# Kernel optimization log

Measured on AMD Instinct MI355X. Metric: run time of the kernel, lower is better.

## Reference

```python
import jax, jax.numpy as jnp
import numpy as np

WS = 7          # window size
SHIFT = 3       # shift size (SW-MSA)
NH = 4          # num heads
EPS = 1e-5      # LayerNorm eps (torch default)


def _rel_pos_index(ws):
    coords = np.stack(np.meshgrid(np.arange(ws), np.arange(ws), indexing='ij'))  # (2, ws, ws)
    cf = coords.reshape(2, -1)                      # (2, ws*ws)
    rel = cf[:, :, None] - cf[:, None, :]           # (2, N, N)
    rel = rel.transpose(1, 2, 0)
    rel[:, :, 0] += ws - 1
    rel[:, :, 1] += ws - 1
    rel[:, :, 0] *= 2 * ws - 1
    return jnp.asarray(rel.sum(-1))                 # (N, N) int

REL_IDX = _rel_pos_index(WS)


def _shift_mask(Hp, Wp, ws, shift):
    """Standard Swin attention mask for shifted windows: (nW, N, N) float32."""
    img = np.zeros((1, Hp, Wp, 1), dtype=np.float32)
    cnt = 0
    sl = (slice(0, -ws), slice(-ws, -shift), slice(-shift, None))
    for h in sl:
        for w in sl:
            img[:, h, w, :] = cnt
            cnt += 1
    win = img.reshape(1, Hp // ws, ws, Wp // ws, ws, 1).transpose(0, 1, 3, 2, 4, 5)
    win = win.reshape(-1, ws * ws)                  # (nW, N)
    m = win[:, None, :] - win[:, :, None]
    return jnp.asarray(np.where(m != 0, -100.0, 0.0).astype(np.float32))


def _ln(x, g, b):
    mu = jnp.mean(x, -1, keepdims=True)
    var = jnp.mean(jnp.square(x - mu), -1, keepdims=True)
    return (x - mu) * jax.lax.rsqrt(var + EPS) * g + b


def _win_partition(x, ws):
    B, H, W, C = x.shape
    x = x.reshape(B, H // ws, ws, W // ws, ws, C).transpose(0, 1, 3, 2, 4, 5)
    return x.reshape(-1, ws * ws, C)


def _win_reverse(w, ws, B, H, W):
    C = w.shape[-1]
    x = w.reshape(B, H // ws, W // ws, ws, ws, C).transpose(0, 1, 3, 2, 4, 5)
    return x.reshape(B, H, W, C)


def setup_inputs() -> dict:
    key = jax.random.key(0)
    ks = jax.random.split(key, 12)
    B, H, W, C = 16, 112, 112, 128
    hid = 4 * C
    std = 0.02
    inp = {
        'x': jax.random.normal(ks[0], (B, H * W, C), jnp.float32),
        'H': H, 'W': W,
        'attn_mask': _shift_mask(H, W, WS, SHIFT),
        'ln1_g': jnp.ones((C,), jnp.float32),
        'ln1_b': jnp.zeros((C,), jnp.float32),
        'qkv_w': jax.random.normal(ks[1], (3 * C, C), jnp.float32) * std,
        'qkv_b': jnp.zeros((3 * C,), jnp.float32),
        'rel_bias_table': jax.random.normal(ks[2], ((2 * WS - 1) ** 2, NH), jnp.float32) * std,
        'proj_w': jax.random.normal(ks[3], (C, C), jnp.float32) * std,
        'proj_b': jnp.zeros((C,), jnp.float32),
        'ln2_g': jnp.ones((C,), jnp.float32),
        'ln2_b': jnp.zeros((C,), jnp.float32),
        'fc1_w': jax.random.normal(ks[4], (hid, C), jnp.float32) * std,
        'fc1_b': jnp.zeros((hid,), jnp.float32),
        'fc2_w': jax.random.normal(ks[5], (C, hid), jnp.float32) * std,
        'fc2_b': jnp.zeros((C,), jnp.float32),
    }
    return inp


def reference(x, H, W, attn_mask, ln1_g, ln1_b, qkv_w, qkv_b, rel_bias_table,
              proj_w, proj_b, ln2_g, ln2_b, fc1_w, fc1_b, fc2_w, fc2_b):
    B, L, C = x.shape
    N = WS * WS
    hd = C // NH
    scale = hd ** -0.5

    shortcut = x
    h = _ln(x, ln1_g, ln1_b).reshape(B, H, W, C)
    # H, W chosen divisible by WS -> no padding branch needed
    h = jnp.roll(h, shift=(-SHIFT, -SHIFT), axis=(1, 2))
    xw = _win_partition(h, WS)                      # (B_, N, C), B_ = B*nW
    B_ = xw.shape[0]
    nW = attn_mask.shape[0]

    qkv = xw @ qkv_w.T + qkv_b                      # (B_, N, 3C)
    qkv = qkv.reshape(B_, N, 3, NH, hd).transpose(2, 0, 3, 1, 4)
    q, k, v = qkv[0], qkv[1], qkv[2]                # (B_, NH, N, hd)

    attn = jnp.einsum('bhnd,bhmd->bhnm', q, k) * scale
    bias = rel_bias_table[REL_IDX]                  # (N, N, NH)
    attn = attn + bias.transpose(2, 0, 1)[None]     # (B_, NH, N, N)
    attn = attn.reshape(B_ // nW, nW, NH, N, N) + attn_mask[None, :, None]
    attn = jax.nn.softmax(attn.reshape(B_, NH, N, N), axis=-1)

    o = jnp.einsum('bhnm,bhmd->bhnd', attn, v)      # (B_, NH, N, hd)
    o = o.transpose(0, 2, 1, 3).reshape(B_, N, C)
    o = o @ proj_w.T + proj_b

    h = _win_reverse(o, WS, B, H, W)
    h = jnp.roll(h, shift=(SHIFT, SHIFT), axis=(1, 2))
    x1 = shortcut + h.reshape(B, L, C)

    f = _ln(x1, ln2_g, ln2_b)
    f = jax.nn.gelu(f @ fc1_w.T + fc1_b, approximate=False)
    f = f @ fc2_w.T + fc2_b
    return x1 + f
```

## Files before the change

### kernel.cpp

```cpp
#include <hip/hip_runtime.h>
#include <hip/hip_bf16.h>
#include <math.h>

#define B_IMG 16
#define HH 112
#define WW_ 112
#define CC 128
#define LL (HH*WW_)
#define BWIN 4096
#define NTOK 49
#define NROWS (BWIN*NTOK)
#define HD 32
#define SCALE 0.1767766952966369f
#define SHIFT_ 3

typedef short bf16x8 __attribute__((ext_vector_type(8)));
typedef float f32x4 __attribute__((ext_vector_type(4)));
typedef unsigned short ushort_t;

__device__ __forceinline__ float wave_sum(float v) {
#pragma unroll
  for (int off = 32; off >= 1; off >>= 1) v += __shfl_xor(v, off, 64);
  return v;
}

__global__ __launch_bounds__(256) void castw_kernel(const float* __restrict__ w,
                                                    __hip_bfloat16* __restrict__ o, int n) {
  int i = blockIdx.x * 256 + threadIdx.x;
  if (i < n) o[i] = __float2bfloat16(w[i]);
}

__global__ __launch_bounds__(256) void prep_bias(const float* __restrict__ table,
                                                 float* __restrict__ biasPad) {
  int idx = blockIdx.x * 256 + threadIdx.x;
  int h = idx >> 12, q = (idx >> 6) & 63, k = idx & 63;
  float v = 0.f;
  if (q < NTOK && k < NTOK) {
    int yi = q / 7, xi = q % 7, yj = k / 7, xj = k % 7;
    v = table[((yi - yj + 6) * 13 + (xi - xj + 6)) * 4 + h];
  }
  biasPad[idx] = v;
}

__global__ __launch_bounds__(256) void prep_mask(const float* __restrict__ mask,
                                                 float* __restrict__ maskPad) {
  int idx = blockIdx.x * 256 + threadIdx.x;
  int pat = idx >> 12, q = (idx >> 6) & 63, k = idx & 63;
  float v = -1e30f;
  if (q < NTOK && k < NTOK) v = mask[pat * (NTOK * NTOK) + q * NTOK + k];
  maskPad[idx] = v;
}

template<bool GATHER>
__global__ __launch_bounds__(256) void ln_kernel(
    const float* __restrict__ X, const float* __restrict__ g,
    const float* __restrict__ b, __hip_bfloat16* __restrict__ Y)
{
  int wid  = threadIdx.x >> 6;
  int lane = threadIdx.x & 63;
  int r = blockIdx.x * 4 + wid;
  size_t src;
  if (GATHER) {
    int win = r / NTOK, n = r % NTOK;
    int bi = win >> 8, wi = win & 255;
    int wh = wi >> 4, wwi = wi & 15;
    int ii = n / 7, jj = n % 7;
    int hp = wh * 7 + ii, wp = wwi * 7 + jj;
    int sh = (hp + SHIFT_) % HH, sw = (wp + SHIFT_) % WW_;
    src = ((size_t)bi * LL + (size_t)sh * WW_ + sw) * CC;
  } else {
    src = (size_t)r * CC;
  }
  float v0 = X[src + lane];
  float v1 = X[src + 64 + lane];
  float mean = wave_sum(v0 + v1) * (1.f / CC);
  float d0 = v0 - mean, d1 = v1 - mean;
  float var = wave_sum(d0 * d0 + d1 * d1) * (1.f / CC);
  float rstd = rsqrtf(var + 1e-5f);
  size_t dst = (size_t)r * CC;
  Y[dst + lane]      = __float2bfloat16(d0 * rstd * g[lane]      + b[lane]);
  Y[dst + 64 + lane] = __float2bfloat16(d1 * rstd * g[lane + 64] + b[lane + 64]);
}

enum { EPI_BIAS = 0, EPI_GELU = 1, EPI_RES = 2, EPI_PROJ = 3 };
#define LDSW 136

#define STAGE_A(KB)                                                              \
  _Pragma("unroll")                                                              \
  for (int p = 0; p < 8; ++p) {                                                  \
    int lin = p * 256 + t;                                                       \
    int row = lin >> 4;                                                          \
    int col = (lin & 15) * 8;                                                    \
    *(uint4*)&As[row * LDSW + col] =                                             \
        *(const uint4*)(A + (size_t)(m0 + row) * K + (KB) + col);                \
  }

#define STAGE_B(NOFF, KB)                                                        \
  _Pragma("unroll")                                                              \
  for (int p = 0; p < 8; ++p) {                                                  \
    int lin = p * 256 + t;                                                       \
    int row = lin >> 4;                                                          \
    int col = (lin & 15) * 8;                                                    \
    *(uint4*)&Bs[row * LDSW + col] =                                             \
        *(const uint4*)(W + (size_t)((NOFF) + row) * K + (KB) + col);            \
  }

#define MFMA_BLOCK                                                               \
  _Pragma("unroll")                                                              \
  for (int ks = 0; ks < 4; ++ks) {                                               \
    int k0 = ks * 32 + quad * 8;                                                 \
    bf16x8 af[4], bf[4];                                                         \
    _Pragma("unroll")                                                            \
    for (int i = 0; i < 4; ++i)                                                  \
      af[i] = *(const bf16x8*)&As[(wr + i * 16 + l16) * LDSW + k0];              \
    _Pragma("unroll")                                                            \
    for (int j = 0; j < 4; ++j)                                                  \
      bf[j] = *(const bf16x8*)&Bs[(wc + j * 16 + l16) * LDSW + k0];              \
    _Pragma("unroll")                                                            \
    for (int i = 0; i < 4; ++i)                                                  \
      _Pragma("unroll")                                                          \
      for (int j = 0; j < 4; ++j)                                                \
        acc[i][j] = __builtin_amdgcn_mfma_f32_16x16x32_bf16(af[i], bf[j],        \
                                                            acc[i][j], 0, 0, 0); \
  }

template<int EPI, int NB, bool LNF>
__global__ __launch_bounds__(256, 2) void gemm_bf16(
    const ushort_t* __restrict__ A, const ushort_t* __restrict__ W,
    const float* __restrict__ bias, const float* __restrict__ aux,
    void* __restrict__ outp, const float* __restrict__ g2,
    const float* __restrict__ b2, __hip_bfloat16* __restrict__ ln_out,
    int N, int K)
{
  __shared__ ushort_t As[128 * LDSW];
  __shared__ ushort_t Bs[128 * LDSW];
  int t = threadIdx.x;
  int lane = t & 63;
  int quad = lane >> 4;
  int l16  = lane & 15;
  int wr = (t >> 7) * 64;
  int wc = ((t >> 6) & 1) * 64;
  int m0 = blockIdx.x * 128;

  f32x4 acc[4][4];

  for (int nb = 0; nb < NB; ++nb) {
    int n_off = (NB == 1) ? blockIdx.y * 128 : nb * 128;
#pragma unroll
    for (int i = 0; i < 4; ++i)
#pragma unroll
      for (int j = 0; j < 4; ++j) acc[i][j] = (f32x4){0.f, 0.f, 0.f, 0.f};

    if (NB == 1) {
      for (int kb = 0; kb < K; kb += 128) {
        if (kb) __syncthreads();
        STAGE_A(kb);
        STAGE_B(n_off, kb);
        __syncthreads();
        MFMA_BLOCK;
      }
    } else {
      if (nb == 0) { STAGE_A(0); STAGE_B(0, 0); }
      __syncthreads();
      MFMA_BLOCK;
      __syncthreads();
      if (nb + 1 < NB) { STAGE_B((nb + 1) * 128, 0); }
    }

    if (EPI == EPI_PROJ) {
      float s[4][4], ss[4][4];
      unsigned rowB[4][4];
#pragma unroll
      for (int i = 0; i < 4; ++i) {
#pragma unroll
        for (int r = 0; r < 4; ++r) {
          s[i][r] = 0.f; ss[i][r] = 0.f;
          int m = m0 + wr + i * 16 + quad * 4 + r;
          int win = m / NTOK, nn = m % NTOK;
          int bi = win >> 8, wi = win & 255;
          int wh = wi >> 4, wwi = wi & 15;
          int ii = nn / 7, jj = nn % 7;
          int hp = wh * 7 + ii, wp = wwi * 7 + jj;
          int oh = (hp + SHIFT_) % HH, ow = (wp + SHIFT_) % WW_;
          unsigned base = ((unsigned)bi * LL + (unsigned)oh * WW_ + ow) * CC;
          rowB[i][r] = base;
#pragma unroll
          for (int j = 0; j < 4; ++j) {
            int n = wc + j * 16 + l16;
            float x1 = aux[base + n] + acc[i][j][r] + bias[n];
            ((float*)outp)[base + n] = x1;
            if (LNF) {
              acc[i][j][r] = x1;
              s[i][r] += x1;
              ss[i][r] = fmaf(x1, x1, ss[i][r]);
            }
          }
        }
      }
      if (LNF) {
#pragma unroll
        for (int i = 0; i < 4; ++i)
#pragma unroll
          for (int r = 0; r < 4; ++r) {
#pragma unroll
            for (int off = 8; off >= 1; off >>= 1) {
              s[i][r]  += __shfl_xor(s[i][r],  off, 64);
              ss[i][r] += __shfl_xor(ss[i][r], off, 64);
            }
          }
        float* red = (float*)As;
        __syncthreads();
        if (l16 == 0) {
#pragma unroll
          for (int i = 0; i < 4; ++i)
#pragma unroll
            for (int r = 0; r < 4; ++r) {
              int ml = wr + i * 16 + quad * 4 + r;
              red[((wc >> 6) * 128 + ml) * 2 + 0] = s[i][r];
              red[((wc >> 6) * 128 + ml) * 2 + 1] = ss[i][r];
            }
        }
        __syncthreads();
#pragma unroll
        for (int i = 0; i < 4; ++i)
#pragma unroll
          for (int r = 0; r < 4; ++r) {
            int ml = wr + i * 16 + quad * 4 + r;
            float st  = red[ml * 2 + 0] + red[(128 + ml) * 2 + 0];
            float sst = red[ml * 2 + 1] + red[(128 + ml) * 2 + 1];
            float mean = st * (1.f / 128.f);
            float var  = sst * (1.f / 128.f) - mean * mean;
            s[i][r]  = mean;
            ss[i][r] = rsqrtf(var + 1e-5f);
          }
#pragma unroll
        for (int i = 0; i < 4; ++i)
#pragma unroll
          for (int r = 0; r < 4; ++r) {
            unsigned base = rowB[i][r];
#pragma unroll
            for (int j = 0; j < 4; ++j) {
              int n = wc + j * 16 + l16;
              float ln = (acc[i][j][r] - s[i][r]) * ss[i][r] * g2[n] + b2[n];
              ln_out[(size_t)base + n] = __float2bfloat16(ln);
            }
          }
      }
    } else {
#pragma unroll
      for (int i = 0; i < 4; ++i) {
#pragma unroll
        for (int j = 0; j < 4; ++j) {
          int n = n_off + wc + j * 16 + l16;
          float bn = bias[n];
#pragma unroll
          for (int reg = 0; reg < 4; ++reg) {
            int m = m0 + wr + i * 16 + quad * 4 + reg;
            float v = acc[i][j][reg] + bn;
            if (EPI == EPI_BIAS) {
              ((__hip_bfloat16*)outp)[(size_t)m * N + n] = __float2bfloat16(v);
            } else if (EPI == EPI_GELU) {
              v = 0.5f * v * (1.f + erff(v * 0.70710678118654752f));
              ((__hip_bfloat16*)outp)[(size_t)m * N + n] = __float2bfloat16(v);
            } else {
              ((float*)outp)[(size_t)m * N + n] = v + aux[(size_t)m * N + n];
            }
          }
        }
      }
    }
  }
}

#define WLDS 6656

__global__ __launch_bounds__(256) void attn_mfma(
    const ushort_t* __restrict__ qkv, const float* __restrict__ maskPad,
    const float* __restrict__ biasPad, __hip_bfloat16* __restrict__ O, int win_off)
{
  __shared__ ushort_t lds[4 * WLDS];
  const int win_l = blockIdx.x;
  const int win_g = win_off + win_l;
  const int h    = threadIdx.x >> 6;
  const int lane = threadIdx.x & 63;
  const int quad = lane >> 4;
  const int l16  = lane & 15;
  ushort_t* wb = lds + h * WLDS;
  ushort_t* Vt = wb + 4608;

  {
    const int tok = lane;
    uint4 z = make_uint4(0u, 0u, 0u, 0u);
    uint4 k0 = z, k1 = z, k2 = z, k3 = z;
    union { uint4 v4[4]; ushort_t u[32]; } vv;
    vv.v4[0] = z; vv.v4[1] = z; vv.v4[2] = z; vv.v4[3] = z;
    if (tok < NTOK) {
      const ushort_t* src = qkv + ((size_t)win_l * NTOK + tok) * 384 + h * HD;
      k0 = *(const uint4*)(src + 128); k1 = *(const uint4*)(src + 136);
      k2 = *(const uint4*)(src + 144); k3 = *(const uint4*)(src + 152);
      vv.v4[0] = *(const uint4*)(src + 256); vv.v4[1] = *(const uint4*)(src + 264);
      vv.v4[2] = *(const uint4*)(src + 272); vv.v4[3] = *(const uint4*)(src + 280);
    }
    *(uint4*)&wb[tok * 40 +  0] = k0;
    *(uint4*)&wb[tok * 40 +  8] = k1;
    *(uint4*)&wb[tok * 40 + 16] = k2;
    *(uint4*)&wb[tok * 40 + 24] = k3;
#pragma unroll
    for (int d = 0; d < 32; ++d) Vt[d * 64 + tok] = vv.u[d];
  }

  bf16x8 qf[4];
  {
    const ushort_t* qb = qkv + (size_t)win_l * NTOK * 384 + h * HD + quad * 8;
#pragma unroll
    for (int i = 0; i < 4; ++i)
      qf[i] = *(const bf16x8*)(qb + (size_t)(i * 16 + l16) * 384);
  }

  f32x4 S[4][4];
#pragma unroll
  for (int i = 0; i < 4; ++i)
#pragma unroll
    for (int j = 0; j < 4; ++j) S[i][j] = (f32x4){0.f, 0.f, 0.f, 0.f};
  bf16x8 kf[4];
#pragma unroll
  for (int j = 0; j < 4; ++j)
    kf[j] = *(const bf16x8*)&wb[(j * 16 + l16) * 40 + quad * 8];
#pragma unroll
  for (int i = 0; i < 4; ++i)
#pragma unroll
    for (int j = 0; j < 4; ++j)
      S[i][j] = __builtin_amdgcn_mfma_f32_16x16x32_bf16(qf[i], kf[j], S[i][j], 0, 0, 0);

  const float* mrow = maskPad + (size_t)(win_g & 255) * 4096;
  const float* brow = biasPad + (size_t)h * 4096;
#pragma unroll
  for (int i = 0; i < 4; ++i)
#pragma unroll
    for (int j = 0; j < 4; ++j)
#pragma unroll
      for (int r = 0; r < 4; ++r) {
        int q = i * 16 + quad * 4 + r;
        int k = j * 16 + l16;
        S[i][j][r] = fmaf(S[i][j][r], SCALE, brow[q * 64 + k] + mrow[q * 64 + k]);
      }

  float inv[4][4];
#pragma unroll
  for (int i = 0; i < 4; ++i)
#pragma unroll
    for (int r = 0; r < 4; ++r) {
      float mx = fmaxf(fmaxf(S[i][0][r], S[i][1][r]), fmaxf(S[i][2][r], S[i][3][r]));
      mx = fmaxf(mx, __shfl_xor(mx, 1, 64));
      mx = fmaxf(mx, __shfl_xor(mx, 2, 64));
      mx = fmaxf(mx, __shfl_xor(mx, 4, 64));
      mx = fmaxf(mx, __shfl_xor(mx, 8, 64));
      float sum = 0.f;
#pragma unroll
      for (int j = 0; j < 4; ++j) {
        float e = __expf(S[i][j][r] - mx);
        S[i][j][r] = e;
        sum += e;
      }
      sum += __shfl_xor(sum, 1, 64);
      sum += __shfl_xor(sum, 2, 64);
      sum += __shfl_xor(sum, 4, 64);
      sum += __shfl_xor(sum, 8, 64);
      inv[i][r] = 1.f / sum;
    }

#pragma unroll
  for (int i = 0; i < 4; ++i)
#pragma unroll
    for (int j = 0; j < 4; ++j)
#pragma unroll
      for (int r = 0; r < 4; ++r) {
        int q = i * 16 + quad * 4 + r;
        int k = j * 16 + l16;
        *(__hip_bfloat16*)&wb[q * 72 + k] = __float2bfloat16(S[i][j][r]);
      }

  f32x4 Oacc[4][2];
#pragma unroll
  for (int i = 0; i < 4; ++i) {
    Oacc[i][0] = (f32x4){0.f, 0.f, 0.f, 0.f};
    Oacc[i][1] = (f32x4){0.f, 0.f, 0.f, 0.f};
  }
  bf16x8 vf[2][2];
#pragma unroll
  for (int ks = 0; ks < 2; ++ks)
#pragma unroll
    for (int jp = 0; jp < 2; ++jp)
      vf[ks][jp] = *(const bf16x8*)&Vt[(jp * 16 + l16) * 64 + ks * 32 + quad * 8];
#pragma unroll
  for (int i = 0; i < 4; ++i)
#pragma unroll
    for (int ks = 0; ks < 2; ++ks) {
      bf16x8 pf = *(const bf16x8*)&wb[(i * 16 + l16) * 72 + ks * 32 + quad * 8];
#pragma unroll
      for (int jp = 0; jp < 2; ++jp)
        Oacc[i][jp] = __builtin_amdgcn_mfma_f32_16x16x32_bf16(pf, vf[ks][jp], Oacc[i][jp], 0, 0, 0);
    }

  __hip_bfloat16* ob = O + ((size_t)win_g * NTOK) * CC + h * HD;
#pragma unroll
  for (int i = 0; i < 4; ++i)
#pragma unroll
    for (int r = 0; r < 4; ++r) {
      int q = i * 16 + quad * 4 + r;
      if (q < NTOK) {
        float sc = inv[i][r];
#pragma unroll
        for (int jp = 0; jp < 2; ++jp)
          ob[(size_t)q * CC + jp * 16 + l16] = __float2bfloat16(Oacc[i][jp][r] * sc);
      }
    }
}

extern "C" void kernel_launch(void* const* d_in, const int* in_sizes, int n_in,
                              void* d_out, int out_size, void* d_ws, size_t ws_size,
                              hipStream_t stream) {
  const float* x        = (const float*)d_in[0];
  const float* attnmask = (const float*)d_in[3];
  const float* ln1_g    = (const float*)d_in[4];
  const float* ln1_b    = (const float*)d_in[5];
  const float* qkv_w    = (const float*)d_in[6];
  const float* qkv_b    = (const float*)d_in[7];
  const float* table    = (const float*)d_in[8];
  const float* proj_w   = (const float*)d_in[9];
  const float* proj_b   = (const float*)d_in[10];
  const float* ln2_g    = (const float*)d_in[11];
  const float* ln2_b    = (const float*)d_in[12];
  const float* fc1_w    = (const float*)d_in[13];
  const float* fc1_b    = (const float*)d_in[14];
  const float* fc2_w    = (const float*)d_in[15];
  const float* fc2_b    = (const float*)d_in[16];
  float* out = (float*)d_out;

  const size_t bufA_elems = (size_t)NROWS * CC;
  const size_t bufB_full  = (size_t)NROWS * 512;
  const size_t bufB_chunk = (size_t)(NROWS / 2) * 384;
  const size_t bufC_elems = (size_t)NROWS * CC;
  const size_t w_elems    = 384*128 + 128*128 + 512*128 + 128*512;
  const size_t tbl_floats = 4 * 4096 + 256 * 4096;
  const size_t need_full  =
      (bufA_elems + bufB_full + bufC_elems + w_elems) * 2 + tbl_floats * 4;
  const bool full = ws_size >= need_full;

  __hip_bfloat16* bufA = (__hip_bfloat16*)d_ws;
  __hip_bfloat16* bufB = bufA + bufA_elems;
  __hip_bfloat16* bufC;
  __hip_bfloat16* wq;
  if (full) {
    bufC = bufB + bufB_full;
    wq   = bufC + bufC_elems;
  } else {
    bufC = nullptr;
    wq   = bufB + bufB_chunk;
  }
  __hip_bfloat16* wp   = wq + 384 * 128;
  __hip_bfloat16* w1   = wp + 128 * 128;
  __hip_bfloat16* w2   = w1 + 512 * 128;
  float* biasPad = (float*)(w2 + 128 * 512);
  float* maskPad = biasPad + 4 * 4096;

  castw_kernel<<<(384 * 128 + 255) / 256, 256, 0, stream>>>(qkv_w, wq, 384 * 128);
  castw_kernel<<<(128 * 128 + 255) / 256, 256, 0, stream>>>(proj_w, wp, 128 * 128);
  castw_kernel<<<(512 * 128 + 255) / 256, 256, 0, stream>>>(fc1_w, w1, 512 * 128);
  castw_kernel<<<(128 * 512 + 255) / 256, 256, 0, stream>>>(fc2_w, w2, 128 * 512);
  prep_bias<<<64, 256, 0, stream>>>(table, biasPad);
  prep_mask<<<4096, 256, 0, stream>>>(attnmask, maskPad);

  ln_kernel<true><<<NROWS / 4, 256, 0, stream>>>(x, ln1_g, ln1_b, bufA);

  if (full) {
    dim3 g(NROWS / 128, 1);
    gemm_bf16<EPI_BIAS, 3, false><<<g, 256, 0, stream>>>(
        (const ushort_t*)bufA, (const ushort_t*)wq, qkv_b, nullptr, bufB,
        nullptr, nullptr, nullptr, 384, 128);
    attn_mfma<<<BWIN, 256, 0, stream>>>((const ushort_t*)bufB, maskPad, biasPad,
                                        bufA, 0);
    gemm_bf16<EPI_PROJ, 1, true><<<g, 256, 0, stream>>>(
        (const ushort_t*)bufA, (const ushort_t*)wp, proj_b, x, out,
        ln2_g, ln2_b, bufC, 128, 128);
    gemm_bf16<EPI_GELU, 4, false><<<g, 256, 0, stream>>>(
        (const ushort_t*)bufC, (const ushort_t*)w1, fc1_b, nullptr, bufB,
        nullptr, nullptr, nullptr, 512, 128);
    gemm_bf16<EPI_RES, 1, false><<<g, 256, 0, stream>>>(
        (const ushort_t*)bufB, (const ushort_t*)w2, fc2_b, out, out,
        nullptr, nullptr, nullptr, 128, 512);
  } else {
    for (int c = 0; c < 2; ++c) {
      const int MC = NROWS / 2;
      const ushort_t* Ain = (const ushort_t*)(bufA + (size_t)c * MC * CC);
      dim3 g(MC / 128, 1);
      gemm_bf16<EPI_BIAS, 3, false><<<g, 256, 0, stream>>>(
          Ain, (const ushort_t*)wq, qkv_b, nullptr, bufB,
          nullptr, nullptr, nullptr, 384, 128);
      attn_mfma<<<2048, 256, 0, stream>>>((const ushort_t*)bufB, maskPad, biasPad,
                                          bufA, c * 2048);
    }
    {
      dim3 g(NROWS / 128, 1);
      gemm_bf16<EPI_PROJ, 1, false><<<g, 256, 0, stream>>>(
          (const ushort_t*)bufA, (const ushort_t*)wp, proj_b, x, out,
          nullptr, nullptr, nullptr, 128, 128);
    }
    ln_kernel<false><<<NROWS / 4, 256, 0, stream>>>(out, ln2_g, ln2_b, bufA);
    for (int c = 0; c < 4; ++c) {
      const int MC = NROWS / 4;
      const ushort_t* Ain = (const ushort_t*)(bufA + (size_t)c * MC * CC);
      float* Oc = out + (size_t)c * MC * CC;
      dim3 g1(MC / 128, 1);
      gemm_bf16<EPI_GELU, 4, false><<<g1, 256, 0, stream>>>(
          Ain, (const ushort_t*)w1, fc1_b, nullptr, bufB,
          nullptr, nullptr, nullptr, 512, 128);
      dim3 g2(MC / 128, 1);
      gemm_bf16<EPI_RES, 1, false><<<g2, 256, 0, stream>>>(
          (const ushort_t*)bufB, (const ushort_t*)w2, fc2_b, Oc, Oc,
          nullptr, nullptr, nullptr, 128, 512);
    }
  }
}
```

Before: 612.6 us.

## Fuse fc1+GELU+fc2 MLP into one kernel and use tanh GELU

Replaces the two separate MLP GEMMs with a single kernel that computes each 128-wide hidden slice in LDS, applies GELU, and immediately accumulates into the fc2 output. This avoids writing and re-reading the 512-wide hidden activation through global memory and shrinks the workspace. It also swaps the exact erf GELU for a tanh approximation built on __expf, which is cheaper but deviates slightly from the reference. The fused kernel uses 64-row tiles with no load/compute overlap and reloads weights per block, so it risks lower MFMA efficiency.

```diff
diff --git a/kernel.cpp b/kernel.cpp
--- a/kernel.cpp
+++ b/kernel.cpp
@@ -22,6 +22,14 @@
 #pragma unroll
   for (int off = 32; off >= 1; off >>= 1) v += __shfl_xor(v, off, 64);
   return v;
+}
+
+__device__ __forceinline__ float gelu_f(float x) {
+  float x3 = x * x * x;
+  float y = 0.7978845608028654f * fmaf(0.044715f, x3, x);
+  float e = __expf(2.f * y);
+  float th = 1.f - 2.f / (e + 1.f);
+  return 0.5f * x * (1.f + th);
 }
 
 __global__ __launch_bounds__(256) void castw_kernel(const float* __restrict__ w,
@@ -260,7 +268,7 @@
             if (EPI == EPI_BIAS) {
               ((__hip_bfloat16*)outp)[(size_t)m * N + n] = __float2bfloat16(v);
             } else if (EPI == EPI_GELU) {
-              v = 0.5f * v * (1.f + erff(v * 0.70710678118654752f));
+              v = gelu_f(v);
               ((__hip_bfloat16*)outp)[(size_t)m * N + n] = __float2bfloat16(v);
             } else {
               ((float*)outp)[(size_t)m * N + n] = v + aux[(size_t)m * N + n];
@@ -270,6 +278,123 @@
       }
     }
   }
+}
+
+__global__ __launch_bounds__(256, 2) void mlp_fused(
+    const ushort_t* __restrict__ A,
+    const ushort_t* __restrict__ W1,
+    const float* __restrict__ b1,
+    const ushort_t* __restrict__ W2,
+    const float* __restrict__ b2,
+    float* __restrict__ out)
+{
+  __shared__ ushort_t As[64 * LDSW];
+  __shared__ ushort_t Bs[128 * LDSW];
+  __shared__ ushort_t Hs[64 * LDSW];
+  int t = threadIdx.x;
+  int lane = t & 63;
+  int quad = lane >> 4;
+  int l16  = lane & 15;
+  int wr = (t >> 7) * 32;
+  int wc = ((t >> 6) & 1) * 64;
+  int m0 = blockIdx.x * 64;
+
+#pragma unroll
+  for (int p = 0; p < 4; ++p) {
+    int lin = p * 256 + t;
+    int row = lin >> 4, col = (lin & 15) * 8;
+    *(uint4*)&As[row * LDSW + col] = *(const uint4*)(A + (size_t)(m0 + row) * 128 + col);
+  }
+
+  f32x4 acc2[2][4];
+#pragma unroll
+  for (int i = 0; i < 2; ++i)
+#pragma unroll
+    for (int j = 0; j < 4; ++j) acc2[i][j] = (f32x4){0.f, 0.f, 0.f, 0.f};
+
+  for (int nb = 0; nb < 4; ++nb) {
+    __syncthreads();
+#pragma unroll
+    for (int p = 0; p < 8; ++p) {
+      int lin = p * 256 + t;
+      int row = lin >> 4, col = (lin & 15) * 8;
+      *(uint4*)&Bs[row * LDSW + col] =
+          *(const uint4*)(W1 + (size_t)(nb * 128 + row) * 128 + col);
+    }
+    __syncthreads();
+    f32x4 acc1[2][4];
+#pragma unroll
+    for (int i = 0; i < 2; ++i)
+#pragma unroll
+      for (int j = 0; j < 4; ++j) acc1[i][j] = (f32x4){0.f, 0.f, 0.f, 0.f};
+#pragma unroll
+    for (int ks = 0; ks < 4; ++ks) {
+      int k0 = ks * 32 + quad * 8;
+      bf16x8 af[2], bf[4];
+#pragma unroll
+      for (int i = 0; i < 2; ++i)
+        af[i] = *(const bf16x8*)&As[(wr + i * 16 + l16) * LDSW + k0];
+#pragma unroll
+      for (int j = 0; j < 4; ++j)
+        bf[j] = *(const bf16x8*)&Bs[(wc + j * 16 + l16) * LDSW + k0];
+#pragma unroll
+      for (int i = 0; i < 2; ++i)
+#pragma unroll
+        for (int j = 0; j < 4; ++j)
+          acc1[i][j] = __builtin_amdgcn_mfma_f32_16x16x32_bf16(af[i], bf[j], acc1[i][j], 0, 0, 0);
+    }
+    __syncthreads();
+#pragma unroll
+    for (int i = 0; i < 2; ++i)
+#pragma unroll
+      for (int j = 0; j < 4; ++j) {
+        int hc = wc + j * 16 + l16;
+        float bn = b1[nb * 128 + hc];
+#pragma unroll
+        for (int r = 0; r < 4; ++r) {
+          int hr = wr + i * 16 + quad * 4 + r;
+          float v = gelu_f(acc1[i][j][r] + bn);
+          *(__hip_bfloat16*)&Hs[hr * LDSW + hc] = __float2bfloat16(v);
+        }
+      }
+#pragma unroll
+    for (int p = 0; p < 8; ++p) {
+      int lin = p * 256 + t;
+      int row = lin >> 4, col = (lin & 15) * 8;
+      *(uint4*)&Bs[row * LDSW + col] =
+          *(const uint4*)(W2 + (size_t)row * 512 + nb * 128 + col);
+    }
+    __syncthreads();
+#pragma unroll
+    for (int ks = 0; ks < 4; ++ks) {
+      int k0 = ks * 32 + quad * 8;
+      bf16x8 hf[2], wf[4];
+#pragma unroll
+      for (int i = 0; i < 2; ++i)
+        hf[i] = *(const bf16x8*)&Hs[(wr + i * 16 + l16) * LDSW + k0];
+#pragma unroll
+      for (int j = 0; j < 4; ++j)
+        wf[j] = *(const bf16x8*)&Bs[(wc + j * 16 + l16) * LDSW + k0];
+#pragma unroll
+      for (int i = 0; i < 2; ++i)
+#pragma unroll
+        for (int j = 0; j < 4; ++j)
+          acc2[i][j] = __builtin_amdgcn_mfma_f32_16x16x32_bf16(hf[i], wf[j], acc2[i][j], 0, 0, 0);
+    }
+  }
+
+#pragma unroll
+  for (int i = 0; i < 2; ++i)
+#pragma unroll
+    for (int j = 0; j < 4; ++j) {
+      int n = wc + j * 16 + l16;
+      float bn = b2[n];
+#pragma unroll
+      for (int r = 0; r < 4; ++r) {
+        int m = m0 + wr + i * 16 + quad * 4 + r;
+        out[(size_t)m * 128 + n] += acc2[i][j][r] + bn;
+      }
+    }
 }
 
 #define WLDS 6656
@@ -438,7 +563,7 @@
   float* out = (float*)d_out;
 
   const size_t bufA_elems = (size_t)NROWS * CC;
-  const size_t bufB_full  = (size_t)NROWS * 512;
+  const size_t bufB_full  = (size_t)NROWS * 384;
   const size_t bufB_chunk = (size_t)(NROWS / 2) * 384;
   const size_t bufC_elems = (size_t)NROWS * CC;
   const size_t w_elems    = 384*128 + 128*128 + 512*128 + 128*512;
@@ -483,12 +608,9 @@
     gemm_bf16<EPI_PROJ, 1, true><<<g, 256, 0, stream>>>(
         (const ushort_t*)bufA, (const ushort_t*)wp, proj_b, x, out,
         ln2_g, ln2_b, bufC, 128, 128);
-    gemm_bf16<EPI_GELU, 4, false><<<g, 256, 0, stream>>>(
-        (const ushort_t*)bufC, (const ushort_t*)w1, fc1_b, nullptr, bufB,
-        nullptr, nullptr, nullptr, 512, 128);
-    gemm_bf16<EPI_RES, 1, false><<<g, 256, 0, stream>>>(
-        (const ushort_t*)bufB, (const ushort_t*)w2, fc2_b, out, out,
-        nullptr, nullptr, nullptr, 128, 512);
+    mlp_fused<<<NROWS / 64, 256, 0, stream>>>(
+        (const ushort_t*)bufC, (const ushort_t*)w1, fc1_b,
+        (const ushort_t*)w2, fc2_b, out);
   } else {
     for (int c = 0; c < 2; ++c) {
       const int MC = NROWS / 2;
```

Measured after the change: 612.6 us. No clear change (+0.0%).

## Fuse output projection, residual add and LayerNorm2 into window attention kernel

Applied to the files above, without the earlier changes.

The attention kernel now stages each window's per-head outputs in LDS, loads the bf16 projection weight into LDS, and runs the projection GEMM with MFMA in the same block. It then adds bias and the residual, writes x1 at the un-shifted positions, and computes LayerNorm2 to emit the bf16 MLP input. This removes the separate projection GEMM launch and the round trip of the attention output through global memory. In exchange, every window block reloads the 128x128 projection weight and does a scattered per-token epilogue, and the fused kernel may use more registers and LDS.

```diff
diff --git a/kernel.cpp b/kernel.cpp
--- a/kernel.cpp
+++ b/kernel.cpp
@@ -274,15 +274,21 @@
 
 #define WLDS 6656
 
+template<bool FUSE_PROJ>
 __global__ __launch_bounds__(256) void attn_mfma(
     const ushort_t* __restrict__ qkv, const float* __restrict__ maskPad,
-    const float* __restrict__ biasPad, __hip_bfloat16* __restrict__ O, int win_off)
+    const float* __restrict__ biasPad, __hip_bfloat16* __restrict__ O,
+    const ushort_t* __restrict__ Wp, const float* __restrict__ pbias,
+    const float* __restrict__ xres, float* __restrict__ out,
+    const float* __restrict__ g2, const float* __restrict__ b2,
+    __hip_bfloat16* __restrict__ ln_out, int win_off)
 {
   __shared__ ushort_t lds[4 * WLDS];
   const int win_l = blockIdx.x;
   const int win_g = win_off + win_l;
-  const int h    = threadIdx.x >> 6;
-  const int lane = threadIdx.x & 63;
+  const int t    = threadIdx.x;
+  const int h    = t >> 6;
+  const int lane = t & 63;
   const int quad = lane >> 4;
   const int l16  = lane & 15;
   ushort_t* wb = lds + h * WLDS;
@@ -402,19 +408,98 @@
         Oacc[i][jp] = __builtin_amdgcn_mfma_f32_16x16x32_bf16(pf, vf[ks][jp], Oacc[i][jp], 0, 0, 0);
     }
 
-  __hip_bfloat16* ob = O + ((size_t)win_g * NTOK) * CC + h * HD;
+  if (!FUSE_PROJ) {
+    __hip_bfloat16* ob = O + ((size_t)win_g * NTOK) * CC + h * HD;
+#pragma unroll
+    for (int i = 0; i < 4; ++i)
+#pragma unroll
+      for (int r = 0; r < 4; ++r) {
+        int q = i * 16 + quad * 4 + r;
+        if (q < NTOK) {
+          float sc = inv[i][r];
+#pragma unroll
+          for (int jp = 0; jp < 2; ++jp)
+            ob[(size_t)q * CC + jp * 16 + l16] = __float2bfloat16(Oacc[i][jp][r] * sc);
+        }
+      }
+    return;
+  }
+
+  __syncthreads();
+  ushort_t* os  = lds;
+  ushort_t* Wps = lds + 64 * LDSW;
 #pragma unroll
   for (int i = 0; i < 4; ++i)
 #pragma unroll
     for (int r = 0; r < 4; ++r) {
       int q = i * 16 + quad * 4 + r;
-      if (q < NTOK) {
-        float sc = inv[i][r];
-#pragma unroll
-        for (int jp = 0; jp < 2; ++jp)
-          ob[(size_t)q * CC + jp * 16 + l16] = __float2bfloat16(Oacc[i][jp][r] * sc);
-      }
-    }
+      float sc = inv[i][r];
+#pragma unroll
+      for (int jp = 0; jp < 2; ++jp)
+        *(__hip_bfloat16*)&os[q * LDSW + h * HD + jp * 16 + l16] =
+            __float2bfloat16(Oacc[i][jp][r] * sc);
+    }
+#pragma unroll
+  for (int p = 0; p < 8; ++p) {
+    int lin = p * 256 + t;
+    int row = lin >> 4;
+    int col = (lin & 15) * 8;
+    *(uint4*)&Wps[row * LDSW + col] = *(const uint4*)(Wp + (size_t)row * 128 + col);
+  }
+  __syncthreads();
+
+  const int wr2 = h * 16;
+  f32x4 pacc[8];
+#pragma unroll
+  for (int j = 0; j < 8; ++j) pacc[j] = (f32x4){0.f, 0.f, 0.f, 0.f};
+#pragma unroll
+  for (int ks = 0; ks < 4; ++ks) {
+    int k0 = ks * 32 + quad * 8;
+    bf16x8 af = *(const bf16x8*)&os[(wr2 + l16) * LDSW + k0];
+#pragma unroll
+    for (int j = 0; j < 8; ++j) {
+      bf16x8 bf = *(const bf16x8*)&Wps[(j * 16 + l16) * LDSW + k0];
+      pacc[j] = __builtin_amdgcn_mfma_f32_16x16x32_bf16(af, bf, pacc[j], 0, 0, 0);
+    }
+  }
+
+#pragma unroll
+  for (int r = 0; r < 4; ++r) {
+    int ml = wr2 + quad * 4 + r;
+    bool live = ml < NTOK;
+    int bi = win_g >> 8, wi = win_g & 255;
+    int wh = wi >> 4, wwi = wi & 15;
+    int ii = ml / 7, jj = ml % 7;
+    int hp = wh * 7 + ii, wp = wwi * 7 + jj;
+    int oh = (hp + SHIFT_) % HH, ow = (wp + SHIFT_) % WW_;
+    size_t base = ((size_t)bi * LL + (size_t)oh * WW_ + ow) * CC;
+    float x1v[8];
+    float s = 0.f, ssum = 0.f;
+#pragma unroll
+    for (int j = 0; j < 8; ++j) {
+      int n = j * 16 + l16;
+      float x1 = xres[base + n] + pacc[j][r] + pbias[n];
+      x1v[j] = x1;
+      if (live) out[base + n] = x1;
+      s += x1;
+      ssum = fmaf(x1, x1, ssum);
+    }
+#pragma unroll
+    for (int off = 8; off >= 1; off >>= 1) {
+      s    += __shfl_xor(s, off, 64);
+      ssum += __shfl_xor(ssum, off, 64);
+    }
+    float mean = s * (1.f / 128.f);
+    float var  = ssum * (1.f / 128.f) - mean * mean;
+    float rstd = rsqrtf(var + 1e-5f);
+    if (live) {
+#pragma unroll
+      for (int j = 0; j < 8; ++j) {
+        int n = j * 16 + l16;
+        ln_out[base + n] = __float2bfloat16((x1v[j] - mean) * rstd * g2[n] + b2[n]);
+      }
+    }
+  }
 }
 
 extern "C" void kernel_launch(void* const* d_in, const int* in_sizes, int n_in,
@@ -478,11 +563,9 @@
     gemm_bf16<EPI_BIAS, 3, false><<<g, 256, 0, stream>>>(
         (const ushort_t*)bufA, (const ushort_t*)wq, qkv_b, nullptr, bufB,
         nullptr, nullptr, nullptr, 384, 128);
-    attn_mfma<<<BWIN, 256, 0, stream>>>((const ushort_t*)bufB, maskPad, biasPad,
-                                        bufA, 0);
-    gemm_bf16<EPI_PROJ, 1, true><<<g, 256, 0, stream>>>(
-        (const ushort_t*)bufA, (const ushort_t*)wp, proj_b, x, out,
-        ln2_g, ln2_b, bufC, 128, 128);
+    attn_mfma<true><<<BWIN, 256, 0, stream>>>(
+        (const ushort_t*)bufB, maskPad, biasPad, nullptr,
+        (const ushort_t*)wp, proj_b, x, out, ln2_g, ln2_b, bufC, 0);
     gemm_bf16<EPI_GELU, 4, false><<<g, 256, 0, stream>>>(
         (const ushort_t*)bufC, (const ushort_t*)w1, fc1_b, nullptr, bufB,
         nullptr, nullptr, nullptr, 512, 128);
@@ -497,8 +580,9 @@
       gemm_bf16<EPI_BIAS, 3, false><<<g, 256, 0, stream>>>(
           Ain, (const ushort_t*)wq, qkv_b, nullptr, bufB,
           nullptr, nullptr, nullptr, 384, 128);
-      attn_mfma<<<2048, 256, 0, stream>>>((const ushort_t*)bufB, maskPad, biasPad,
-                                          bufA, c * 2048);
+      attn_mfma<false><<<2048, 256, 0, stream>>>(
+          (const ushort_t*)bufB, maskPad, biasPad, bufA,
+          nullptr, nullptr, nullptr, nullptr, nullptr, nullptr, nullptr, c * 2048);
     }
     {
       dim3 g(NROWS / 128, 1);
```

Measured after the change: 694.2 us. 1.13x slower.
